# Kernel tuning notes

Hardware: AMD Instinct MI355X
Metric: run time of the kernel (lower is better)

Reference implementation:

```python
import jax, jax.numpy as jnp
import numpy as np

B, C, H, W = 2, 64, 48, 48
NH = 8
EPS = 1e-5


def conv2d(x, w, b=None, pad=0):
    out = jax.lax.conv_general_dilated(x, w, (1, 1), [(pad, pad), (pad, pad)],
                                       dimension_numbers=('NCHW', 'OIHW', 'NCHW'))
    return out if b is None else out + b[None, :, None, None]


def bn2d(x, g, b, m, v):
    # eval-mode BatchNorm2d with running stats
    return (x - m[None, :, None, None]) * (g / jnp.sqrt(v + EPS))[None, :, None, None] + b[None, :, None, None]


def ln(x, g, b):
    mu = x.mean(-1, keepdims=True)
    var = ((x - mu) ** 2).mean(-1, keepdims=True)
    return (x - mu) / jnp.sqrt(var + EPS) * g + b


def _forward(x, y, pconv_w, pconv_b, bnd_g, bnd_b, bnd_m, bnd_v,
             lnx_g, lnx_b, lny_g, lny_b, lnz_g, lnz_b,
             k_w, k_b, qv_w, qv_b, proj_w, proj_b,
             c2w1, c2b1, c2bn1_g, c2bn1_b, c2bn1_m, c2bn1_v,
             c2w2, c2b2, c2bn2_g, c2bn2_b, c2bn2_m, c2bn2_v,
             bn2_g, bn2_b, bn2_m, bn2_v,
             f1w, fbn1_g, fbn1_b, fbn1_m, fbn1_v,
             f2w, fbn2_g, fbn2_b, fbn2_m, fbn2_v,
             f3w, f3b):
    Bq, Cq, Hq, Wq = x.shape
    N = Hq * Wq
    hd = Cq // NH
    scale = hd ** -0.5
    xy = conv2d(jnp.concatenate([x, y], 1), pconv_w, pconv_b, pad=0)
    xb = bn2d(x, bnd_g, bnd_b, bnd_m, bnd_v)
    yb = bn2d(y, bnd_g, bnd_b, bnd_m, bnd_v)
    xyb = bn2d(xy, bnd_g, bnd_b, bnd_m, bnd_v)
    sc1 = xb.reshape(Bq, Cq, N).transpose(0, 2, 1)  # [B,N,C]
    sd1 = yb.reshape(Bq, Cq, N).transpose(0, 2, 1)
    xl = ln(sc1, lnx_g, lnx_b)
    yl = ln(sd1, lny_g, lny_b)
    zl = ln(xyb.reshape(Bq, Cq, N).transpose(0, 2, 1), lnz_g, lnz_b)

    def qv_heads(t):
        qv = (t @ qv_w.T + qv_b).reshape(Bq, N, 2, NH, hd)
        return qv[:, :, 0].transpose(0, 2, 1, 3), qv[:, :, 1].transpose(0, 2, 1, 3)

    x_q, x_v = qv_heads(xl)
    y_q, y_v = qv_heads(yl)
    k = (zl @ k_w.T + k_b).reshape(Bq, N, NH, hd).transpose(0, 2, 1, 3)  # [B,H,N,hd]
    attn1 = jnp.einsum('bhnd,bhmd->bhnm', x_q, k) * scale
    attn2 = jnp.einsum('bhnd,bhmd->bhnm', y_q, k) * scale
    attn = jax.nn.softmax(attn1 * attn2, axis=-1)  # product of two score maps
    xo = jnp.einsum('bhnm,bhmd->bhnd', attn, x_v).transpose(0, 2, 1, 3).reshape(Bq, N, Cq) @ proj_w.T + proj_b
    yo = jnp.einsum('bhnm,bhmd->bhnd', attn, y_v).transpose(0, 2, 1, 3).reshape(Bq, N, Cq) @ proj_w.T + proj_b
    xo = (xo + sc1).transpose(0, 2, 1).reshape(Bq, Cq, Hq, Wq)
    yo = (yo + sd1).transpose(0, 2, 1).reshape(Bq, Cq, Hq, Wq)

    def conv2_block(t):  # shared-weight conv2 applied to both branches
        h = jax.nn.relu(bn2d(conv2d(t, c2w1, c2b1, pad=1), c2bn1_g, c2bn1_b, c2bn1_m, c2bn1_v))
        return jax.nn.relu(bn2d(conv2d(h, c2w2, c2b2, pad=1), c2bn2_g, c2bn2_b, c2bn2_m, c2bn2_v))

    xo = conv2_block(xo) + xo
    yo = conv2_block(yo) + yo
    cat = jnp.concatenate([xo + yo, xo * yo], 1)  # [B,2C,H,W]
    f = bn2d(cat, bn2_g, bn2_b, bn2_m, bn2_v)
    f = jax.nn.relu(bn2d(conv2d(f, f1w, None, pad=1), fbn1_g, fbn1_b, fbn1_m, fbn1_v))
    f = jax.nn.relu(bn2d(conv2d(f, f2w, None, pad=1), fbn2_g, fbn2_b, fbn2_m, fbn2_v))
    f = conv2d(f, f3w, f3b, pad=0)
    return cat + f


def setup_inputs() -> dict:
    ks = iter(jax.random.split(jax.random.key(0), 64))

    def nrm(shape, s=0.05):
        return jax.random.normal(next(ks), shape, jnp.float32) * s

    def bn_params(c):
        return (1.0 + nrm((c,)), nrm((c,)), nrm((c,)),
                jax.random.uniform(next(ks), (c,), jnp.float32, 0.5, 1.5))

    d = {}
    d['x'] = jax.random.normal(next(ks), (B, C, H, W), jnp.float32)
    d['y'] = jax.random.normal(next(ks), (B, C, H, W), jnp.float32)
    d['pconv_w'] = nrm((C, 2 * C, 1, 1)); d['pconv_b'] = nrm((C,))
    d['bnd_g'], d['bnd_b'], d['bnd_m'], d['bnd_v'] = bn_params(C)
    d['lnx_g'] = 1.0 + nrm((C,)); d['lnx_b'] = nrm((C,))
    d['lny_g'] = 1.0 + nrm((C,)); d['lny_b'] = nrm((C,))
    d['lnz_g'] = 1.0 + nrm((C,)); d['lnz_b'] = nrm((C,))
    d['k_w'] = nrm((C, C)); d['k_b'] = nrm((C,))
    d['qv_w'] = nrm((2 * C, C)); d['qv_b'] = nrm((2 * C,))
    d['proj_w'] = nrm((C, C)); d['proj_b'] = nrm((C,))
    d['c2w1'] = nrm((C, C, 3, 3)); d['c2b1'] = nrm((C,))
    d['c2bn1_g'], d['c2bn1_b'], d['c2bn1_m'], d['c2bn1_v'] = bn_params(C)
    d['c2w2'] = nrm((C, C, 3, 3)); d['c2b2'] = nrm((C,))
    d['c2bn2_g'], d['c2bn2_b'], d['c2bn2_m'], d['c2bn2_v'] = bn_params(C)
    d['bn2_g'], d['bn2_b'], d['bn2_m'], d['bn2_v'] = bn_params(2 * C)
    d['f1w'] = nrm((2 * C, 2 * C, 3, 3))
    d['fbn1_g'], d['fbn1_b'], d['fbn1_m'], d['fbn1_v'] = bn_params(2 * C)
    d['f2w'] = nrm((2 * C, 2 * C, 3, 3))
    d['fbn2_g'], d['fbn2_b'], d['fbn2_m'], d['fbn2_v'] = bn_params(2 * C)
    d['f3w'] = nrm((2 * C, 2 * C, 1, 1)); d['f3b'] = nrm((2 * C,))
    return d


def reference(x, y, pconv_w, pconv_b, bnd_g, bnd_b, bnd_m, bnd_v,
              lnx_g, lnx_b, lny_g, lny_b, lnz_g, lnz_b,
              k_w, k_b, qv_w, qv_b, proj_w, proj_b,
              c2w1, c2b1, c2bn1_g, c2bn1_b, c2bn1_m, c2bn1_v,
              c2w2, c2b2, c2bn2_g, c2bn2_b, c2bn2_m, c2bn2_v,
              bn2_g, bn2_b, bn2_m, bn2_v,
              f1w, fbn1_g, fbn1_b, fbn1_m, fbn1_v,
              f2w, fbn2_g, fbn2_b, fbn2_m, fbn2_v,
              f3w, f3b):
    return _forward(x, y, pconv_w, pconv_b, bnd_g, bnd_b, bnd_m, bnd_v,
                    lnx_g, lnx_b, lny_g, lny_b, lnz_g, lnz_b,
                    k_w, k_b, qv_w, qv_b, proj_w, proj_b,
                    c2w1, c2b1, c2bn1_g, c2bn1_b, c2bn1_m, c2bn1_v,
                    c2w2, c2b2, c2bn2_g, c2bn2_b, c2bn2_m, c2bn2_v,
                    bn2_g, bn2_b, bn2_m, bn2_v,
                    f1w, fbn1_g, fbn1_b, fbn1_m, fbn1_v,
                    f2w, fbn2_g, fbn2_b, fbn2_m, fbn2_v,
                    f3w, f3b)
```

## Files before the change

### kernel.cpp

```cpp
#include <hip/hip_runtime.h>
#include <hip/hip_bf16.h>

#define B_   2
#define C_   64
#define H_   48
#define W_   48
#define N_   (H_*W_)
#define NH_  8
#define HD_  8
#define EPS_ 1e-5f
#define S2_  0.125f
#define LOG2E_ 1.44269504f
#define FS_  (S2_ * LOG2E_)
#define S_   ((size_t)B_ * C_ * N_)
#define CN_  ((size_t)C_ * N_)
#define ROWP_ 52
#define CBUF_ (8 * ROWP_)
#define XTSZ_ ((N_ + 2 * W_) * 128)

typedef unsigned short u16;
typedef __attribute__((ext_vector_type(8))) short short8v;
typedef __attribute__((ext_vector_type(4))) float f32x4;
union F8 { uint4 u4; short8v s; unsigned int w[4]; };

__device__ __forceinline__ float wsum64(float v) {
#pragma unroll
  for (int o = 32; o > 0; o >>= 1) v += __shfl_xor(v, o, 64);
  return v;
}

__device__ __forceinline__ float ln_val(float t, float g, float b) {
  float mu  = wsum64(t) * (1.0f / 64.0f);
  float d   = t - mu;
  float var = wsum64(d * d) * (1.0f / 64.0f);
  return d * rsqrtf(var + EPS_) * g + b;
}

__device__ __forceinline__ u16 f2bf(float x) {
  union { float f; unsigned int u; } a; a.f = x;
  unsigned int r = a.u + 0x7fffu + ((a.u >> 16) & 1u);
  return (u16)(r >> 16);
}

__global__ __launch_bounds__(1024) void k_pre(
    const float* __restrict__ x, const float* __restrict__ y,
    const float* __restrict__ pw, const float* __restrict__ pb,
    const float* g, const float* bb, const float* m, const float* v,
    const float* lnxg, const float* lnxb,
    const float* lnyg, const float* lnyb,
    const float* lnzg, const float* lnzb,
    float* __restrict__ xl, float* __restrict__ yl, float* __restrict__ zl) {
  __shared__ float4 pwT[32][64];
  __shared__ float xs[16][64], ys[16][64];
  int w = threadIdx.x >> 6, c = threadIdx.x & 63;
  for (int idx = threadIdx.x; idx < 2048; idx += 1024) {
    int cc = idx & 63, i4 = idx >> 6;
    pwT[i4][cc] = *(const float4*)(pw + (size_t)cc * 2 * C_ + i4 * 4);
  }
  int row = blockIdx.x * 16 + w;
  int b = row / N_, n = row % N_;
  float xv = x[(size_t)(b * C_ + c) * N_ + n];
  float yv = y[(size_t)(b * C_ + c) * N_ + n];
  xs[w][c] = xv; ys[w][c] = yv;
  __syncthreads();
  const float4* xw = (const float4*)xs[w];
  const float4* yw = (const float4*)ys[w];
  float acc = pb[c];
#pragma unroll
  for (int t = 0; t < 16; ++t) {
    float4 a = xw[t], wv = pwT[t][c];
    acc += a.x * wv.x + a.y * wv.y + a.z * wv.z + a.w * wv.w;
  }
#pragma unroll
  for (int t = 0; t < 16; ++t) {
    float4 a = yw[t], wv = pwT[16 + t][c];
    acc += a.x * wv.x + a.y * wv.y + a.z * wv.z + a.w * wv.w;
  }
  float s  = g[c] * rsqrtf(v[c] + EPS_);
  float sh = bb[c] - m[c] * s;
  float tx = xv * s + sh;
  xl[(size_t)row * C_ + c] = ln_val(tx, lnxg[c], lnxb[c]);
  float ty = yv * s + sh;
  yl[(size_t)row * C_ + c] = ln_val(ty, lnyg[c], lnyb[c]);
  float tz = acc * s + sh;
  zl[(size_t)row * C_ + c] = ln_val(tz, lnzg[c], lnzb[c]);
}

__global__ __launch_bounds__(64) void k_qvk(
    const float* __restrict__ xl, const float* __restrict__ yl,
    const float* __restrict__ zl,
    const float* __restrict__ qvw, const float* __restrict__ qvb,
    const float* __restrict__ kw, const float* __restrict__ kb,
    u16* __restrict__ qxb, u16* __restrict__ qyb,
    u16* __restrict__ kbf, u16* __restrict__ vt) {
  int l = threadIdx.x;
  int part = blockIdx.y >> 2;
  int j0 = (blockIdx.y & 3) * 16;
  int row = blockIdx.x * 64 + l;
  int b = row / N_, n = row % N_;
  const float* inp = (part < 2) ? xl : (part < 4) ? yl : zl;
  float4 in[16];
  const float4* ir = (const float4*)(inp + (size_t)row * C_);
#pragma unroll
  for (int t = 0; t < 16; ++t) in[t] = ir[t];

  const float* wb   = (part == 4) ? kw : qvw;
  const float* bias = (part == 4) ? kb : qvb;
  int joff = (part == 1 || part == 3) ? 64 : 0;

  if (part == 1 || part == 3) {
    int vbase = (part == 1) ? 0 : 8;
#pragma unroll
    for (int jj = 0; jj < 16; ++jj) {
      int j = j0 + jj;
      const float4* wr = (const float4*)(wb + (size_t)(joff + j) * C_);
      float acc = bias[joff + j];
#pragma unroll
      for (int t = 0; t < 16; ++t) {
        float4 a = in[t], wv = wr[t];
        acc += a.x * wv.x + a.y * wv.y + a.z * wv.z + a.w * wv.w;
      }
      int h = j >> 3, d = j & 7;
      vt[((size_t)((b * NH_ + h) * 16 + vbase + d)) * N_ + n] = f2bf(acc);
    }
  } else {
    u16* dst = (part == 0) ? qxb : (part == 2) ? qyb : kbf;
#pragma unroll
    for (int gg = 0; gg < 2; ++gg) {
      int h = (j0 >> 3) + gg;
      union { uint4 u4; u16 s[8]; } pk;
#pragma unroll
      for (int d = 0; d < 8; ++d) {
        int j = h * 8 + d;
        const float4* wr = (const float4*)(wb + (size_t)(joff + j) * C_);
        float acc = bias[joff + j];
#pragma unroll
        for (int t = 0; t < 16; ++t) {
          float4 a = in[t], wv = wr[t];
          acc += a.x * wv.x + a.y * wv.y + a.z * wv.z + a.w * wv.w;
        }
        if (part == 0) acc *= FS_;
        pk.s[d] = f2bf(acc);
      }
      *(uint4*)(dst + ((size_t)(b * NH_ + h) * N_ + n) * 8) = pk.u4;
    }
  }
}

__global__ __launch_bounds__(128, 5) void k_attn8(
    const u16* __restrict__ qx, const u16* __restrict__ qy,
    const u16* __restrict__ kk, const u16* __restrict__ vt,
    float* __restrict__ outx, float* __restrict__ outy) {
  __shared__ float sAcc[2][4][64];
  __shared__ float sL[2][16];
  int qt = blockIdx.x, bh = blockIdx.y;
  int tid = threadIdx.x;
  int lane = tid & 63;
  int wave = tid >> 6;
  int l15 = lane & 15;
  int q0 = qt * 16;

  F8 qxf, qyf;
  size_t qoff = ((size_t)bh * N_ + q0 + l15) * 8;
  qxf.u4 = *(const uint4*)(qx + qoff);
  qyf.u4 = *(const uint4*)(qy + qoff);
  if (lane >= 16) {
    qxf.u4 = make_uint4(0u, 0u, 0u, 0u);
    qyf.u4 = make_uint4(0u, 0u, 0u, 0u);
  }

  int key0 = wave * (N_ / 2);
  const uint4* kp = (const uint4*)(kk + (size_t)bh * N_ * 8) + key0 + l15;
  const uint4* vp = (const uint4*)(vt + ((size_t)bh * 16 + l15) * N_ + key0)
                    + (lane >> 4);
  int addr0 = (((lane >> 4) & 1) * 32 + l15) * 4;
  int addr1 = addr0 + 64;
  int thi = lane >> 5;

  f32x4 acc = {0.f, 0.f, 0.f, 0.f};
  const f32x4 z4 = {0.f, 0.f, 0.f, 0.f};
  float lsum = 0.f;

  F8 ka, kb2, vf;
  ka.u4 = kp[0]; kb2.u4 = kp[16]; vf.u4 = *vp;
  for (int c = 0; c < 36; ++c) {
    F8 kaC = ka, kbC = kb2, vfC = vf;
    kp += 32; vp += 4;
    ka.u4 = kp[0]; kb2.u4 = kp[16]; vf.u4 = *vp;

    f32x4 s1a = __builtin_amdgcn_mfma_f32_16x16x32_bf16(kaC.s, qxf.s, z4, 0, 0, 0);
    f32x4 s2a = __builtin_amdgcn_mfma_f32_16x16x32_bf16(kaC.s, qyf.s, z4, 0, 0, 0);
    f32x4 s1b = __builtin_amdgcn_mfma_f32_16x16x32_bf16(kbC.s, qxf.s, z4, 0, 0, 0);
    f32x4 s2b = __builtin_amdgcn_mfma_f32_16x16x32_bf16(kbC.s, qyf.s, z4, 0, 0, 0);

    float p00 = exp2f(s1a[0] * s2a[0]), p01 = exp2f(s1a[1] * s2a[1]);
    float p02 = exp2f(s1a[2] * s2a[2]), p03 = exp2f(s1a[3] * s2a[3]);
    float p10 = exp2f(s1b[0] * s2b[0]), p11 = exp2f(s1b[1] * s2b[1]);
    float p12 = exp2f(s1b[2] * s2b[2]), p13 = exp2f(s1b[3] * s2b[3]);
    lsum += ((p00 + p01) + (p02 + p03)) + ((p10 + p11) + (p12 + p13));

    unsigned int pk00, pk10, pk01, pk11;
    asm("v_cvt_pk_bf16_f32 %0, %1, %2" : "=v"(pk00) : "v"(p00), "v"(p01));
    asm("v_cvt_pk_bf16_f32 %0, %1, %2" : "=v"(pk10) : "v"(p02), "v"(p03));
    asm("v_cvt_pk_bf16_f32 %0, %1, %2" : "=v"(pk01) : "v"(p10), "v"(p11));
    asm("v_cvt_pk_bf16_f32 %0, %1, %2" : "=v"(pk11) : "v"(p12), "v"(p13));

    int b00 = __builtin_amdgcn_ds_bpermute(addr0, (int)pk00);
    int b01 = __builtin_amdgcn_ds_bpermute(addr0, (int)pk01);
    int b10 = __builtin_amdgcn_ds_bpermute(addr0, (int)pk10);
    int b11 = __builtin_amdgcn_ds_bpermute(addr0, (int)pk11);
    int c00 = __builtin_amdgcn_ds_bpermute(addr1, (int)pk00);
    int c01 = __builtin_amdgcn_ds_bpermute(addr1, (int)pk01);
    int c10 = __builtin_amdgcn_ds_bpermute(addr1, (int)pk10);
    int c11 = __builtin_amdgcn_ds_bpermute(addr1, (int)pk11);

    F8 pf;
    pf.w[0] = (unsigned int)(thi ? b01 : b00);
    pf.w[1] = (unsigned int)(thi ? b11 : b10);
    pf.w[2] = (unsigned int)(thi ? c01 : c00);
    pf.w[3] = (unsigned int)(thi ? c11 : c10);
    acc = __builtin_amdgcn_mfma_f32_16x16x32_bf16(pf.s, vfC.s, acc, 0, 0, 0);
  }

  lsum += __shfl_xor(lsum, 16, 64);
  lsum += __shfl_xor(lsum, 32, 64);
  if (lane < 16) sL[wave][lane] = lsum;
#pragma unroll
  for (int r = 0; r < 4; ++r) sAcc[wave][r][lane] = acc[r];
  __syncthreads();
  if (wave == 0) {
    float Linv = 1.f / (sL[0][l15] + sL[1][l15]);
    int b = bh >> 3, h = bh & 7;
    int d = l15 & 7;
    float* ob = (l15 < 8) ? outx : outy;
    size_t cbase = (size_t)b * N_ * C_ + (size_t)h * 8 + d;
#pragma unroll
    for (int r = 0; r < 4; ++r) {
      int qrow = 4 * (lane >> 4) + r;
      float li = __shfl(Linv, qrow, 64);
      float a = sAcc[0][r][lane] + sAcc[1][r][lane];
      ob[cbase + (size_t)(q0 + qrow) * C_] = a * li;
    }
  }
}

__global__ __launch_bounds__(64) void k_proj3(
    const float* __restrict__ attbase,
    const float* __restrict__ x, const float* __restrict__ y,
    const float* bg, const float* bb2, const float* bm, const float* bv,
    const float* __restrict__ pw, const float* __restrict__ pbias,
    float* __restrict__ outbase) {
  __shared__ float attT[64][66];
  int tid = threadIdx.x;
  int p0 = blockIdx.x * 64;
  int c0 = blockIdx.y * 2;
  int z = blockIdx.z;
  int branch = z >> 1, b = z & 1;
  const float* att = attbase + branch * S_ + (size_t)b * N_ * C_;
  for (int r = 0; r < 64; ++r)
    attT[tid][r] = att[(size_t)(p0 + r) * C_ + tid];
  __syncthreads();
  int p = p0 + tid;
  const float* w0 = pw + (size_t)c0 * C_;
  const float* w1 = w0 + C_;
  float a0 = pbias[c0], a1 = pbias[c0 + 1];
#pragma unroll 8
  for (int c = 0; c < C_; ++c) {
    float av = attT[c][tid];
    a0 += av * w0[c];
    a1 += av * w1[c];
  }
  float s0  = bg[c0] * rsqrtf(bv[c0] + EPS_);
  float sh0 = bb2[c0] - bm[c0] * s0;
  float s1  = bg[c0+1] * rsqrtf(bv[c0+1] + EPS_);
  float sh1 = bb2[c0+1] - bm[c0+1] * s1;
  const float* xin = branch ? y : x;
  float r0 = xin[((size_t)b * C_ + c0) * N_ + p];
  float r1 = xin[((size_t)b * C_ + c0 + 1) * N_ + p];
  size_t o = (size_t)z * CN_ + (size_t)c0 * N_ + p;
  outbase[o]      = a0 + r0 * s0 + sh0;
  outbase[o + N_] = a1 + r1 * s1 + sh1;
}

template<int CIN, int CIPB>
__device__ __forceinline__ void conv_core3(
    const float* __restrict__ ib, const float* __restrict__ w,
    int c0, int ci0, int p0, int tid, float (*bufs)[CBUF_],
    float4& A0, float4& A1) {
  const float* w0r = w + ((size_t)c0 * CIN + ci0) * 9;
  const float* w1r = w0r + (size_t)CIN * 9;
  int p  = p0 + tid * 4;
  int yy0 = p0 / W_;
  int yy = p / W_, x0 = p - yy * W_;
  int lr = yy - yy0;
  bool okL = x0 > 0, okR = x0 + 4 < W_;

  int rf0 = tid / 12, cf0 = tid - rf0 * 12;
  int gy0 = yy0 - 1 + rf0;
  int rf1 = (64 + tid) / 12, cf1 = (64 + tid) - rf1 * 12;
  int gy1 = yy0 - 1 + rf1;
  bool v0 = (unsigned)gy0 < (unsigned)H_;
  bool v1 = (tid < 32) && ((unsigned)gy1 < (unsigned)H_);
  int o0 = gy0 * W_ + cf0 * 4;
  int o1 = gy1 * W_ + cf1 * 4;
  int lo0 = rf0 * ROWP_ + cf0 * 4;
  int lo1 = rf1 * ROWP_ + cf1 * 4;
  const float4 zz = make_float4(0.f, 0.f, 0.f, 0.f);

  {
    const float* s = ib + (size_t)ci0 * N_;
    float4 ga = v0 ? *(const float4*)(s + o0) : zz;
    *(float4*)(&bufs[0][lo0]) = ga;
    if (tid < 32) {
      float4 gb = v1 ? *(const float4*)(s + o1) : zz;
      *(float4*)(&bufs[0][lo1]) = gb;
    }
  }
  float wc[18];
#pragma unroll
  for (int i = 0; i < 9; ++i) { wc[i] = w0r[i]; wc[9 + i] = w1r[i]; }

#pragma unroll 2
  for (int ci = 0; ci < CIPB; ++ci) {
    float4 ga = zz, gb = zz;
    float wn[18];
    if (ci + 1 < CIPB) {
      const float* s = ib + (size_t)(ci0 + ci + 1) * N_;
      ga = v0 ? *(const float4*)(s + o0) : zz;
      gb = v1 ? *(const float4*)(s + o1) : zz;
      const float* nw0 = w0r + (ci + 1) * 9;
      const float* nw1 = w1r + (ci + 1) * 9;
#pragma unroll
      for (int i = 0; i < 9; ++i) { wn[i] = nw0[i]; wn[9 + i] = nw1[i]; }
    }
    const float* bc = bufs[ci & 1];
#pragma unroll
    for (int ky = 0; ky < 3; ++ky) {
      int base = (lr + ky) * ROWP_ + x0;
      float4 mid = *(const float4*)(bc + base);
      float l = okL ? bc[base - 1] : 0.f;
      float r = okR ? bc[base + 4] : 0.f;
      float u0 = wc[ky*3], u1 = wc[ky*3+1], u2 = wc[ky*3+2];
      float t0 = wc[9+ky*3], t1 = wc[9+ky*3+1], t2 = wc[9+ky*3+2];
      A0.x += l     * u0 + mid.x * u1 + mid.y * u2;
      A0.y += mid.x * u0 + mid.y * u1 + mid.z * u2;
      A0.z += mid.y * u0 + mid.z * u1 + mid.w * u2;
      A0.w += mid.z * u0 + mid.w * u1 + r     * u2;
      A1.x += l     * t0 + mid.x * t1 + mid.y * t2;
      A1.y += mid.x * t0 + mid.y * t1 + mid.z * t2;
      A1.z += mid.y * t0 + mid.z * t1 + mid.w * t2;
      A1.w += mid.z * t0 + mid.w * t1 + r     * t2;
    }
    if (ci + 1 < CIPB) {
      float* d = bufs[(ci + 1) & 1];
      *(float4*)(&d[lo0]) = ga;
      if (tid < 32) *(float4*)(&d[lo1]) = gb;
#pragma unroll
      for (int i = 0; i < 18; ++i) wc[i] = wn[i];
    }
  }
}

template<int MODE>
__global__ __launch_bounds__(128) void k_convf(
    const float* __restrict__ inA, const float* __restrict__ inB,
    const float* __restrict__ w, const float* __restrict__ cb,
    const float* g, const float* b2, const float* m, const float* v,
    const float* __restrict__ resid,
    float* __restrict__ oA, float* __restrict__ oB) {
  __shared__ float lds[2 * 2 * CBUF_ + 512];
  int tid = threadIdx.x, wave = tid >> 6, lane = tid & 63;
  int tile = blockIdx.x, c0 = blockIdx.y * 2, img = blockIdx.z;
  const float* ib = (img < 2) ? inA + (size_t)img * CN_
                              : inB + (size_t)(img - 2) * CN_;
  float (*mybufs)[CBUF_] = (float(*)[CBUF_])(lds + wave * 2 * CBUF_);
  float* comb = lds + 4 * CBUF_;
  float4 A0 = make_float4(0.f,0.f,0.f,0.f);
  float4 A1 = make_float4(0.f,0.f,0.f,0.f);
  conv_core3<C_, C_/2>(ib, w, c0, wave * (C_/2), tile * 256, lane, mybufs,
                       A0, A1);
  float* cw = comb + wave * 256 + lane * 4;
  *(float4*)cw = wave ? A0 : A1;
  __syncthreads();
  {
    int c = c0 + wave;
    const float4 other = *(const float4*)(comb + (1 - wave) * 256 + lane * 4);
    float4 a = wave ? other : A0;
    float4 d = wave ? A1 : other;
    int p = tile * 256 + lane * 4;
    float s  = g[c] * rsqrtf(v[c] + EPS_);
    float sh = b2[c] - m[c] * s;
    float bias = cb[c];
    float4 r;
    r.x = fmaxf((a.x + d.x + bias) * s + sh, 0.f);
    r.y = fmaxf((a.y + d.y + bias) * s + sh, 0.f);
    r.z = fmaxf((a.z + d.z + bias) * s + sh, 0.f);
    r.w = fmaxf((a.w + d.w + bias) * s + sh, 0.f);
    size_t off = (size_t)img * CN_ + (size_t)c * N_ + p;
    if (MODE == 0) {
      float* ob = (img < 2) ? oA + off : oB + off - 2 * CN_;
      *(float4*)ob = r;
    } else {
      float4 rr = *(const float4*)(resid + off);
      r.x += rr.x; r.y += rr.y; r.z += rr.z; r.w += rr.w;
      *(float4*)(oA + off) = r;
    }
  }
}

__global__ void k_catbn(const float* __restrict__ o2,
                        const float* __restrict__ g, const float* __restrict__ b2,
                        const float* __restrict__ m, const float* __restrict__ v,
                        float* __restrict__ cat, u16* __restrict__ xt1) {
  int t = blockIdx.x * 256 + threadIdx.x;
  int p4 = t * 4;
  int n  = p4 % N_;
  int c2 = (p4 / N_) % (2 * C_);
  int b  = p4 / (2 * C_ * N_);
  int c  = c2 & 63;
  float4 X = *(const float4*)(o2 + (size_t)b * CN_ + (size_t)c * N_ + n);
  float4 Y = *(const float4*)(o2 + (size_t)(2 + b) * CN_ + (size_t)c * N_ + n);
  float4 val;
  if (c2 < C_) val = make_float4(X.x + Y.x, X.y + Y.y, X.z + Y.z, X.w + Y.w);
  else         val = make_float4(X.x * Y.x, X.y * Y.y, X.z * Y.z, X.w * Y.w);
  size_t co = ((size_t)b * 2 * C_ + c2) * N_ + n;
  *(float4*)(cat + co) = val;
  float s  = g[c2] * rsqrtf(v[c2] + EPS_);
  float sh = b2[c2] - m[c2] * s;
  u16* xb = xt1 + (size_t)b * XTSZ_ + (size_t)(W_ + n) * 128 + c2;
  xb[0]       = f2bf(val.x * s + sh);
  xb[128]     = f2bf(val.y * s + sh);
  xb[256]     = f2bf(val.z * s + sh);
  xb[384]     = f2bf(val.w * s + sh);
}

__global__ void k_zg(u16* __restrict__ xt1, u16* __restrict__ xt2) {
  int idx = blockIdx.x * 256 + threadIdx.x;
  if (idx >= 24576) return;
  int r = idx / 3072, o = idx - r * 3072;
  u16* base = (r & 4) ? xt2 : xt1;
  int b = (r >> 1) & 1, hi = r & 1;
  unsigned int* p = (unsigned int*)(base + (size_t)b * XTSZ_
                                    + (hi ? (size_t)(W_ + N_) * 128 : 0));
  p[o] = 0u;
}

__global__ void k_wcvt(const float* __restrict__ w1,
                       const float* __restrict__ w2,
                       u16* __restrict__ wb1, u16* __restrict__ wb2) {
  int idx = blockIdx.x * 256 + threadIdx.x;
  if (idx >= 2 * 147456) return;
  int layer = idx / 147456, rem = idx - layer * 147456;
  int t = rem / 16384, r2 = rem - t * 16384;
  int co = r2 >> 7, ci = r2 & 127;
  const float* w = layer ? w2 : w1;
  u16* ob = layer ? wb2 : wb1;
  ob[rem] = f2bf(w[(size_t)co * 1152 + ci * 9 + t]);
}

template<int MODE>
__global__ __launch_bounds__(64) void k_fmma(
    const u16* __restrict__ xt, const u16* __restrict__ wb,
    const float* g, const float* b2, const float* m, const float* v,
    u16* __restrict__ xto, float* __restrict__ fo) {
  int l = threadIdx.x;
  int c = l & 15, gg = l >> 4;
  int px0 = blockIdx.x * 16;
  int ct0 = blockIdx.y * 16;
  int b = blockIdx.z;
  int x0 = px0 % W_;
  bool mL = (x0 == 0) && (c == 0);
  bool mR = (x0 == 32) && (c == 15);
  const u16* xb = xt + (size_t)b * XTSZ_ + (size_t)W_ * 128;
  const u16* aw = wb + (size_t)(ct0 + c) * 128 + gg * 8;

  f32x4 acc = {0.f, 0.f, 0.f, 0.f};
#pragma unroll
  for (int cb = 0; cb < 4; ++cb) {
#pragma unroll
    for (int t = 0; t < 9; ++t) {
      const int dx = t % 3 - 1, dy = t / 3 - 1;
      F8 af, bf;
      af.u4 = *(const uint4*)(aw + t * 16384 + cb * 32);
      int px = px0 + c + dx + dy * W_;
      px = max(px, -W_);
      bf.u4 = *(const uint4*)(xb + (ptrdiff_t)px * 128 + cb * 32 + gg * 8);
      bool msk = (dx < 0 && mL) || (dx > 0 && mR);
      if (msk) bf.u4 = make_uint4(0u, 0u, 0u, 0u);
      acc = __builtin_amdgcn_mfma_f32_16x16x32_bf16(af.s, bf.s, acc, 0, 0, 0);
    }
  }
  int px = px0 + c;
  if (MODE == 0) {
    union { ushort4 u; u16 s[4]; } pk;
#pragma unroll
    for (int r = 0; r < 4; ++r) {
      int cout = ct0 + 4 * gg + r;
      float s = g[cout] * rsqrtf(v[cout] + EPS_);
      float sh = b2[cout] - m[cout] * s;
      pk.s[r] = f2bf(fmaxf(acc[r] * s + sh, 0.f));
    }
    *(ushort4*)(xto + (size_t)b * XTSZ_ + (size_t)(W_ + px) * 128
                + ct0 + 4 * gg) = pk.u;
  } else {
#pragma unroll
    for (int r = 0; r < 4; ++r) {
      int cout = ct0 + 4 * gg + r;
      fo[(size_t)b * S_ + (size_t)cout * N_ + px] = acc[r];
    }
  }
}

__global__ __launch_bounds__(64) void k_final3(
    const float* __restrict__ ff, size_t strideF,
    const float* __restrict__ g2, const float* __restrict__ b2,
    const float* __restrict__ m2, const float* __restrict__ v2,
    const float* __restrict__ cat,
    const float* __restrict__ w, const float* __restrict__ fb,
    float* __restrict__ out) {
  __shared__ float fsc[2 * C_], fsh[2 * C_];
  for (int j = threadIdx.x; j < 2 * C_; j += 64) {
    float s = g2[j] * rsqrtf(v2[j] + EPS_);
    fsc[j] = s;
    fsh[j] = b2[j] - m2[j] * s;
  }
  __syncthreads();
  int p = blockIdx.x * 128 + threadIdx.x * 2;
  int c0 = blockIdx.y * 2;
  int b = blockIdx.z;
  const float* fr = ff + (size_t)b * strideF;
  const float* wr0 = w + (size_t)c0 * 2 * C_;
  const float* wr1 = wr0 + 2 * C_;
  float a00 = fb[c0], a01 = a00;
  float a10 = fb[c0 + 1], a11 = a10;
#pragma unroll 4
  for (int j = 0; j < 2 * C_; ++j) {
    float2 fa = *(const float2*)(fr + (size_t)j * N_ + p);
    float s = fsc[j], sh = fsh[j];
    float f0 = fmaxf(fa.x * s + sh, 0.f);
    float f1 = fmaxf(fa.y * s + sh, 0.f);
    float wv0 = wr0[j], wv1 = wr1[j];
    a00 += wv0 * f0; a01 += wv0 * f1;
    a10 += wv1 * f0; a11 += wv1 * f1;
  }
  size_t o = ((size_t)b * 2 * C_ + c0) * N_ + p;
  float2 cv0 = *(const float2*)(cat + o);
  float2 cv1 = *(const float2*)(cat + o + N_);
  *(float2*)(out + o)      = make_float2(a00 + cv0.x, a01 + cv0.y);
  *(float2*)(out + o + N_) = make_float2(a10 + cv1.x, a11 + cv1.y);
}

extern "C" void kernel_launch(void* const* d_in, const int* in_sizes, int n_in,
                              void* d_out, int out_size, void* d_ws, size_t ws_size,
                              hipStream_t stream) {
  const float* x       = (const float*)d_in[0];
  const float* y       = (const float*)d_in[1];
  const float* pconv_w = (const float*)d_in[2];
  const float* pconv_b = (const float*)d_in[3];
  const float* bnd_g = (const float*)d_in[4];
  const float* bnd_b = (const float*)d_in[5];
  const float* bnd_m = (const float*)d_in[6];
  const float* bnd_v = (const float*)d_in[7];
  const float* lnx_g = (const float*)d_in[8];
  const float* lnx_b = (const float*)d_in[9];
  const float* lny_g = (const float*)d_in[10];
  const float* lny_b = (const float*)d_in[11];
  const float* lnz_g = (const float*)d_in[12];
  const float* lnz_b = (const float*)d_in[13];
  const float* k_w   = (const float*)d_in[14];
  const float* k_b   = (const float*)d_in[15];
  const float* qv_w  = (const float*)d_in[16];
  const float* qv_b  = (const float*)d_in[17];
  const float* proj_w = (const float*)d_in[18];
  const float* proj_b = (const float*)d_in[19];
  const float* c2w1  = (const float*)d_in[20];
  const float* c2b1  = (const float*)d_in[21];
  const float* c2bn1_g = (const float*)d_in[22];
  const float* c2bn1_b = (const float*)d_in[23];
  const float* c2bn1_m = (const float*)d_in[24];
  const float* c2bn1_v = (const float*)d_in[25];
  const float* c2w2  = (const float*)d_in[26];
  const float* c2b2  = (const float*)d_in[27];
  const float* c2bn2_g = (const float*)d_in[28];
  const float* c2bn2_b = (const float*)d_in[29];
  const float* c2bn2_m = (const float*)d_in[30];
  const float* c2bn2_v = (const float*)d_in[31];
  const float* bn2_g = (const float*)d_in[32];
  const float* bn2_b = (const float*)d_in[33];
  const float* bn2_m = (const float*)d_in[34];
  const float* bn2_v = (const float*)d_in[35];
  const float* f1w   = (const float*)d_in[36];
  const float* fbn1_g = (const float*)d_in[37];
  const float* fbn1_b = (const float*)d_in[38];
  const float* fbn1_m = (const float*)d_in[39];
  const float* fbn1_v = (const float*)d_in[40];
  const float* f2w   = (const float*)d_in[41];
  const float* fbn2_g = (const float*)d_in[42];
  const float* fbn2_b = (const float*)d_in[43];
  const float* fbn2_m = (const float*)d_in[44];
  const float* fbn2_v = (const float*)d_in[45];
  const float* f3w   = (const float*)d_in[46];
  const float* f3b   = (const float*)d_in[47];

  float* ws = (float*)d_ws;
  float* sl0 = ws + 0 * S_;
  float* sl1 = ws + 1 * S_;
  float* sl2 = ws + 2 * S_;
  float* sl3 = ws + 3 * S_;
  float* sl4 = ws + 4 * S_;
  float* sl5 = ws + 5 * S_;
  float* sl7 = ws + 7 * S_;
  u16* xt1  = (u16*)sl5;
  u16* xt2  = (u16*)sl0;
  u16* wbf1 = (u16*)sl7;
  u16* wbf2 = wbf1 + 9 * 16384;
  float* f2o = sl5;

  k_pre<<<B_ * N_ / 16, 1024, 0, stream>>>(x, y, pconv_w, pconv_b,
                                    bnd_g, bnd_b, bnd_m, bnd_v,
                                    lnx_g, lnx_b, lny_g, lny_b, lnz_g, lnz_b,
                                    sl1, sl2, sl3);
  u16* qxb = (u16*)(ws + 4 * S_);
  u16* qyb = qxb + (size_t)B_ * NH_ * N_ * 8;
  u16* kbf = (u16*)sl5;
  u16* vtb = (u16*)(ws + 6 * S_);
  {
    dim3 g(B_ * N_ / 64, 20);
    k_qvk<<<g, 64, 0, stream>>>(sl1, sl2, sl3, qv_w, qv_b, k_w, k_b,
                                qxb, qyb, kbf, vtb);
  }
  {
    dim3 g(N_ / 16, B_ * NH_);
    k_attn8<<<g, 128, 0, stream>>>(qxb, qyb, kbf, vtb, sl1, sl2);
  }
  {
    dim3 g(36, C_ / 2, 2 * B_);
    k_proj3<<<g, 64, 0, stream>>>(sl1, x, y, bnd_g, bnd_b, bnd_m, bnd_v,
                                  proj_w, proj_b, sl3);
  }
  {
    dim3 g(9, C_ / 2, 4);
    k_convf<0><<<g, 128, 0, stream>>>(sl3, sl3 + 2 * CN_, c2w1, c2b1,
        c2bn1_g, c2bn1_b, c2bn1_m, c2bn1_v, sl3, sl0, sl7);
  }
  {
    dim3 g(9, C_ / 2, 4);
    k_convf<1><<<g, 128, 0, stream>>>(sl0, sl7, c2w2, c2b2,
        c2bn2_g, c2bn2_b, c2bn2_m, c2bn2_v, sl3, sl1, sl1);
  }
  k_wcvt<<<1152, 256, 0, stream>>>(f1w, f2w, wbf1, wbf2);
  k_catbn<<<576, 256, 0, stream>>>(sl1, bn2_g, bn2_b, bn2_m, bn2_v,
                                   sl3, xt1);
  k_zg<<<96, 256, 0, stream>>>(xt1, xt2);
  {
    dim3 g(N_ / 16, 8, B_);
    k_fmma<0><<<g, 64, 0, stream>>>(xt1, wbf1,
        fbn1_g, fbn1_b, fbn1_m, fbn1_v, xt2, nullptr);
    k_fmma<1><<<g, 64, 0, stream>>>(xt2, wbf2,
        nullptr, nullptr, nullptr, nullptr, nullptr, f2o);
  }
  {
    dim3 g(18, C_, B_);
    k_final3<<<g, 64, 0, stream>>>(f2o, S_,
                                   fbn2_g, fbn2_b, fbn2_m, fbn2_v,
                                   sl3, f3w, f3b, (float*)d_out);
  }
}
```

Before: 357.1 us.

## Run conv2 3x3 convolutions as bf16 MFMA implicit GEMMs instead of FP32 direct conv

Replaces the FP32 direct-convolution kernels for the two 64-channel 3x3 convs with the existing bf16 MFMA implicit-GEMM kernel, adding modes for bias+BN+ReLU and for the residual output. The projection kernel now also writes a padded bf16 channels-last copy of its output for the first conv, and weight conversion for all four convs is merged into one kernel launched early. This targets the FP32 FMA cost of the direct conv, at the price of bf16 rounding in the conv path and more workspace aliasing.

```diff
diff --git a/kernel.cpp b/kernel.cpp
--- a/kernel.cpp
+++ b/kernel.cpp
@@ -14,9 +14,8 @@
 #define FS_  (S2_ * LOG2E_)
 #define S_   ((size_t)B_ * C_ * N_)
 #define CN_  ((size_t)C_ * N_)
-#define ROWP_ 52
-#define CBUF_ (8 * ROWP_)
-#define XTSZ_ ((N_ + 2 * W_) * 128)
+#define XTSZ_ ((size_t)(N_ + 2 * W_) * 128)
+#define XTSC_ ((size_t)(N_ + 2 * W_) * 64)
 
 typedef unsigned short u16;
 typedef __attribute__((ext_vector_type(8))) short short8v;
@@ -244,12 +243,12 @@
   }
 }
 
-__global__ __launch_bounds__(64) void k_proj3(
+__global__ __launch_bounds__(64) void k_proj4(
     const float* __restrict__ attbase,
     const float* __restrict__ x, const float* __restrict__ y,
     const float* bg, const float* bb2, const float* bm, const float* bv,
     const float* __restrict__ pw, const float* __restrict__ pbias,
-    float* __restrict__ outbase) {
+    float* __restrict__ outbase, u16* __restrict__ xt0) {
   __shared__ float attT[64][66];
   int tid = threadIdx.x;
   int p0 = blockIdx.x * 64;
@@ -277,135 +276,13 @@
   const float* xin = branch ? y : x;
   float r0 = xin[((size_t)b * C_ + c0) * N_ + p];
   float r1 = xin[((size_t)b * C_ + c0 + 1) * N_ + p];
+  float v0 = a0 + r0 * s0 + sh0;
+  float v1 = a1 + r1 * s1 + sh1;
   size_t o = (size_t)z * CN_ + (size_t)c0 * N_ + p;
-  outbase[o]      = a0 + r0 * s0 + sh0;
-  outbase[o + N_] = a1 + r1 * s1 + sh1;
-}
-
-template<int CIN, int CIPB>
-__device__ __forceinline__ void conv_core3(
-    const float* __restrict__ ib, const float* __restrict__ w,
-    int c0, int ci0, int p0, int tid, float (*bufs)[CBUF_],
-    float4& A0, float4& A1) {
-  const float* w0r = w + ((size_t)c0 * CIN + ci0) * 9;
-  const float* w1r = w0r + (size_t)CIN * 9;
-  int p  = p0 + tid * 4;
-  int yy0 = p0 / W_;
-  int yy = p / W_, x0 = p - yy * W_;
-  int lr = yy - yy0;
-  bool okL = x0 > 0, okR = x0 + 4 < W_;
-
-  int rf0 = tid / 12, cf0 = tid - rf0 * 12;
-  int gy0 = yy0 - 1 + rf0;
-  int rf1 = (64 + tid) / 12, cf1 = (64 + tid) - rf1 * 12;
-  int gy1 = yy0 - 1 + rf1;
-  bool v0 = (unsigned)gy0 < (unsigned)H_;
-  bool v1 = (tid < 32) && ((unsigned)gy1 < (unsigned)H_);
-  int o0 = gy0 * W_ + cf0 * 4;
-  int o1 = gy1 * W_ + cf1 * 4;
-  int lo0 = rf0 * ROWP_ + cf0 * 4;
-  int lo1 = rf1 * ROWP_ + cf1 * 4;
-  const float4 zz = make_float4(0.f, 0.f, 0.f, 0.f);
-
-  {
-    const float* s = ib + (size_t)ci0 * N_;
-    float4 ga = v0 ? *(const float4*)(s + o0) : zz;
-    *(float4*)(&bufs[0][lo0]) = ga;
-    if (tid < 32) {
-      float4 gb = v1 ? *(const float4*)(s + o1) : zz;
-      *(float4*)(&bufs[0][lo1]) = gb;
-    }
-  }
-  float wc[18];
-#pragma unroll
-  for (int i = 0; i < 9; ++i) { wc[i] = w0r[i]; wc[9 + i] = w1r[i]; }
-
-#pragma unroll 2
-  for (int ci = 0; ci < CIPB; ++ci) {
-    float4 ga = zz, gb = zz;
-    float wn[18];
-    if (ci + 1 < CIPB) {
-      const float* s = ib + (size_t)(ci0 + ci + 1) * N_;
-      ga = v0 ? *(const float4*)(s + o0) : zz;
-      gb = v1 ? *(const float4*)(s + o1) : zz;
-      const float* nw0 = w0r + (ci + 1) * 9;
-      const float* nw1 = w1r + (ci + 1) * 9;
-#pragma unroll
-      for (int i = 0; i < 9; ++i) { wn[i] = nw0[i]; wn[9 + i] = nw1[i]; }
-    }
-    const float* bc = bufs[ci & 1];
-#pragma unroll
-    for (int ky = 0; ky < 3; ++ky) {
-      int base = (lr + ky) * ROWP_ + x0;
-      float4 mid = *(const float4*)(bc + base);
-      float l = okL ? bc[base - 1] : 0.f;
-      float r = okR ? bc[base + 4] : 0.f;
-      float u0 = wc[ky*3], u1 = wc[ky*3+1], u2 = wc[ky*3+2];
-      float t0 = wc[9+ky*3], t1 = wc[9+ky*3+1], t2 = wc[9+ky*3+2];
-      A0.x += l     * u0 + mid.x * u1 + mid.y * u2;
-      A0.y += mid.x * u0 + mid.y * u1 + mid.z * u2;
-      A0.z += mid.y * u0 + mid.z * u1 + mid.w * u2;
-      A0.w += mid.z * u0 + mid.w * u1 + r     * u2;
-      A1.x += l     * t0 + mid.x * t1 + mid.y * t2;
-      A1.y += mid.x * t0 + mid.y * t1 + mid.z * t2;
-      A1.z += mid.y * t0 + mid.z * t1 + mid.w * t2;
-      A1.w += mid.z * t0 + mid.w * t1 + r     * t2;
-    }
-    if (ci + 1 < CIPB) {
-      float* d = bufs[(ci + 1) & 1];
-      *(float4*)(&d[lo0]) = ga;
-      if (tid < 32) *(float4*)(&d[lo1]) = gb;
-#pragma unroll
-      for (int i = 0; i < 18; ++i) wc[i] = wn[i];
-    }
-  }
-}
-
-template<int MODE>
-__global__ __launch_bounds__(128) void k_convf(
-    const float* __restrict__ inA, const float* __restrict__ inB,
-    const float* __restrict__ w, const float* __restrict__ cb,
-    const float* g, const float* b2, const float* m, const float* v,
-    const float* __restrict__ resid,
-    float* __restrict__ oA, float* __restrict__ oB) {
-  __shared__ float lds[2 * 2 * CBUF_ + 512];
-  int tid = threadIdx.x, wave = tid >> 6, lane = tid & 63;
-  int tile = blockIdx.x, c0 = blockIdx.y * 2, img = blockIdx.z;
-  const float* ib = (img < 2) ? inA + (size_t)img * CN_
-                              : inB + (size_t)(img - 2) * CN_;
-  float (*mybufs)[CBUF_] = (float(*)[CBUF_])(lds + wave * 2 * CBUF_);
-  float* comb = lds + 4 * CBUF_;
-  float4 A0 = make_float4(0.f,0.f,0.f,0.f);
-  float4 A1 = make_float4(0.f,0.f,0.f,0.f);
-  conv_core3<C_, C_/2>(ib, w, c0, wave * (C_/2), tile * 256, lane, mybufs,
-                       A0, A1);
-  float* cw = comb + wave * 256 + lane * 4;
-  *(float4*)cw = wave ? A0 : A1;
-  __syncthreads();
-  {
-    int c = c0 + wave;
-    const float4 other = *(const float4*)(comb + (1 - wave) * 256 + lane * 4);
-    float4 a = wave ? other : A0;
-    float4 d = wave ? A1 : other;
-    int p = tile * 256 + lane * 4;
-    float s  = g[c] * rsqrtf(v[c] + EPS_);
-    float sh = b2[c] - m[c] * s;
-    float bias = cb[c];
-    float4 r;
-    r.x = fmaxf((a.x + d.x + bias) * s + sh, 0.f);
-    r.y = fmaxf((a.y + d.y + bias) * s + sh, 0.f);
-    r.z = fmaxf((a.z + d.z + bias) * s + sh, 0.f);
-    r.w = fmaxf((a.w + d.w + bias) * s + sh, 0.f);
-    size_t off = (size_t)img * CN_ + (size_t)c * N_ + p;
-    if (MODE == 0) {
-      float* ob = (img < 2) ? oA + off : oB + off - 2 * CN_;
-      *(float4*)ob = r;
-    } else {
-      float4 rr = *(const float4*)(resid + off);
-      r.x += rr.x; r.y += rr.y; r.z += rr.z; r.w += rr.w;
-      *(float4*)(oA + off) = r;
-    }
-  }
+  outbase[o]      = v0;
+  outbase[o + N_] = v1;
+  unsigned int pv = ((unsigned int)f2bf(v1) << 16) | (unsigned int)f2bf(v0);
+  *(unsigned int*)(xt0 + (size_t)z * XTSC_ + (size_t)(W_ + p) * 64 + c0) = pv;
 }
 
 __global__ void k_catbn(const float* __restrict__ o2,
@@ -428,41 +305,62 @@
   float s  = g[c2] * rsqrtf(v[c2] + EPS_);
   float sh = b2[c2] - m[c2] * s;
   u16* xb = xt1 + (size_t)b * XTSZ_ + (size_t)(W_ + n) * 128 + c2;
-  xb[0]       = f2bf(val.x * s + sh);
-  xb[128]     = f2bf(val.y * s + sh);
-  xb[256]     = f2bf(val.z * s + sh);
-  xb[384]     = f2bf(val.w * s + sh);
-}
-
-__global__ void k_zg(u16* __restrict__ xt1, u16* __restrict__ xt2) {
+  xb[0]   = f2bf(val.x * s + sh);
+  xb[128] = f2bf(val.y * s + sh);
+  xb[256] = f2bf(val.z * s + sh);
+  xb[384] = f2bf(val.w * s + sh);
+}
+
+__global__ void k_zg(u16* __restrict__ b0, u16* __restrict__ b1,
+                     int nimg, int cinc) {
+  int gsz = W_ * cinc / 2;
+  int pbt = nimg * 2 * gsz;
   int idx = blockIdx.x * 256 + threadIdx.x;
-  if (idx >= 24576) return;
-  int r = idx / 3072, o = idx - r * 3072;
-  u16* base = (r & 4) ? xt2 : xt1;
-  int b = (r >> 1) & 1, hi = r & 1;
-  unsigned int* p = (unsigned int*)(base + (size_t)b * XTSZ_
-                                    + (hi ? (size_t)(W_ + N_) * 128 : 0));
-  p[o] = 0u;
+  if (idx >= 2 * pbt) return;
+  u16* base = (idx < pbt) ? b0 : b1;
+  int r = idx % pbt;
+  int img = r / (2 * gsz);
+  int r2 = r % (2 * gsz);
+  int hi = r2 / gsz, o = r2 % gsz;
+  size_t xts = (size_t)(N_ + 2 * W_) * cinc;
+  ((unsigned int*)(base + (size_t)img * xts
+                   + (hi ? (size_t)(W_ + N_) * cinc : 0)))[o] = 0u;
 }
 
 __global__ void k_wcvt(const float* __restrict__ w1,
                        const float* __restrict__ w2,
-                       u16* __restrict__ wb1, u16* __restrict__ wb2) {
+                       const float* __restrict__ cw1,
+                       const float* __restrict__ cw2,
+                       u16* __restrict__ wb) {
   int idx = blockIdx.x * 256 + threadIdx.x;
-  if (idx >= 2 * 147456) return;
-  int layer = idx / 147456, rem = idx - layer * 147456;
-  int t = rem / 16384, r2 = rem - t * 16384;
-  int co = r2 >> 7, ci = r2 & 127;
-  const float* w = layer ? w2 : w1;
-  u16* ob = layer ? wb2 : wb1;
-  ob[rem] = f2bf(w[(size_t)co * 1152 + ci * 9 + t]);
+  if (idx >= 368640) return;
+  if (idx < 294912) {
+    int layer = idx / 147456, rem = idx - layer * 147456;
+    int t = rem / 16384, r2 = rem - t * 16384;
+    int co = r2 >> 7, ci = r2 & 127;
+    wb[idx] = f2bf((layer ? w2 : w1)[(size_t)co * 1152 + ci * 9 + t]);
+  } else {
+    int k = idx - 294912;
+    int layer = k / 36864, rem = k - layer * 36864;
+    int t = rem / 4096, r2 = rem - t * 4096;
+    int co = r2 >> 6, ci = r2 & 63;
+    wb[idx] = f2bf((layer ? cw2 : cw1)[(size_t)co * 576 + ci * 9 + t]);
+  }
 }
 
 template<int MODE>
 __global__ __launch_bounds__(64) void k_fmma(
     const u16* __restrict__ xt, const u16* __restrict__ wb,
+    const float* __restrict__ cbias,
     const float* g, const float* b2, const float* m, const float* v,
+    const float* __restrict__ resid,
     u16* __restrict__ xto, float* __restrict__ fo) {
+  constexpr int CIN  = (MODE >= 2) ? 64 : 128;
+  constexpr int NCB  = CIN / 32;
+  constexpr int COUT = (MODE >= 2) ? 64 : 128;
+  constexpr int TS   = CIN * COUT;
+  constexpr size_t XTS = (size_t)(N_ + 2 * W_) * CIN;
+  constexpr size_t XTSO = (size_t)(N_ + 2 * W_) * COUT;
   int l = threadIdx.x;
   int c = l & 15, gg = l >> 4;
   int px0 = blockIdx.x * 16;
@@ -471,42 +369,53 @@
   int x0 = px0 % W_;
   bool mL = (x0 == 0) && (c == 0);
   bool mR = (x0 == 32) && (c == 15);
-  const u16* xb = xt + (size_t)b * XTSZ_ + (size_t)W_ * 128;
-  const u16* aw = wb + (size_t)(ct0 + c) * 128 + gg * 8;
+  const u16* xb = xt + (size_t)b * XTS + (size_t)W_ * CIN;
+  const u16* aw = wb + (size_t)(ct0 + c) * CIN + gg * 8;
 
   f32x4 acc = {0.f, 0.f, 0.f, 0.f};
 #pragma unroll
-  for (int cb = 0; cb < 4; ++cb) {
+  for (int cb = 0; cb < NCB; ++cb) {
 #pragma unroll
     for (int t = 0; t < 9; ++t) {
       const int dx = t % 3 - 1, dy = t / 3 - 1;
       F8 af, bf;
-      af.u4 = *(const uint4*)(aw + t * 16384 + cb * 32);
+      af.u4 = *(const uint4*)(aw + t * TS + cb * 32);
       int px = px0 + c + dx + dy * W_;
       px = max(px, -W_);
-      bf.u4 = *(const uint4*)(xb + (ptrdiff_t)px * 128 + cb * 32 + gg * 8);
+      bf.u4 = *(const uint4*)(xb + (ptrdiff_t)px * CIN + cb * 32 + gg * 8);
       bool msk = (dx < 0 && mL) || (dx > 0 && mR);
       if (msk) bf.u4 = make_uint4(0u, 0u, 0u, 0u);
       acc = __builtin_amdgcn_mfma_f32_16x16x32_bf16(af.s, bf.s, acc, 0, 0, 0);
     }
   }
   int px = px0 + c;
-  if (MODE == 0) {
+  if (MODE == 0 || MODE == 2) {
     union { ushort4 u; u16 s[4]; } pk;
 #pragma unroll
     for (int r = 0; r < 4; ++r) {
       int cout = ct0 + 4 * gg + r;
+      float a = acc[r] + (MODE == 2 ? cbias[cout] : 0.f);
       float s = g[cout] * rsqrtf(v[cout] + EPS_);
       float sh = b2[cout] - m[cout] * s;
-      pk.s[r] = f2bf(fmaxf(acc[r] * s + sh, 0.f));
-    }
-    *(ushort4*)(xto + (size_t)b * XTSZ_ + (size_t)(W_ + px) * 128
+      pk.s[r] = f2bf(fmaxf(a * s + sh, 0.f));
+    }
+    *(ushort4*)(xto + (size_t)b * XTSO + (size_t)(W_ + px) * COUT
                 + ct0 + 4 * gg) = pk.u;
-  } else {
+  } else if (MODE == 1) {
 #pragma unroll
     for (int r = 0; r < 4; ++r) {
       int cout = ct0 + 4 * gg + r;
       fo[(size_t)b * S_ + (size_t)cout * N_ + px] = acc[r];
+    }
+  } else {
+#pragma unroll
+    for (int r = 0; r < 4; ++r) {
+      int cout = ct0 + 4 * gg + r;
+      float a = acc[r] + cbias[cout];
+      float s = g[cout] * rsqrtf(v[cout] + EPS_);
+      float sh = b2[cout] - m[cout] * s;
+      size_t off = (size_t)b * CN_ + (size_t)cout * N_ + px;
+      fo[off] = fmaxf(a * s + sh, 0.f) + resid[off];
     }
   }
 }
@@ -603,23 +512,28 @@
   const float* f3b   = (const float*)d_in[47];
 
   float* ws = (float*)d_ws;
-  float* sl0 = ws + 0 * S_;
   float* sl1 = ws + 1 * S_;
   float* sl2 = ws + 2 * S_;
   float* sl3 = ws + 3 * S_;
-  float* sl4 = ws + 4 * S_;
   float* sl5 = ws + 5 * S_;
-  float* sl7 = ws + 7 * S_;
-  u16* xt1  = (u16*)sl5;
-  u16* xt2  = (u16*)sl0;
-  u16* wbf1 = (u16*)sl7;
-  u16* wbf2 = wbf1 + 9 * 16384;
+  u16* xtC0 = (u16*)sl5;
+  u16* xtC1 = (u16*)ws;
+  u16* xtF1 = (u16*)(ws + 3 * S_ / 2);
+  u16* xtF2 = (u16*)ws;
+  float* xo4 = sl3;
+  float* o2  = sl5;
   float* f2o = sl5;
+  u16* wb   = (u16*)(ws + 7 * S_);
+  u16* wbf1 = wb;
+  u16* wbf2 = wb + 147456;
+  u16* wbc1 = wb + 294912;
+  u16* wbc2 = wb + 331776;
 
   k_pre<<<B_ * N_ / 16, 1024, 0, stream>>>(x, y, pconv_w, pconv_b,
                                     bnd_g, bnd_b, bnd_m, bnd_v,
                                     lnx_g, lnx_b, lny_g, lny_b, lnz_g, lnz_b,
                                     sl1, sl2, sl3);
+  k_wcvt<<<1440, 256, 0, stream>>>(f1w, f2w, c2w1, c2w2, wb);
   u16* qxb = (u16*)(ws + 4 * S_);
   u16* qyb = qxb + (size_t)B_ * NH_ * N_ * 8;
   u16* kbf = (u16*)sl5;
@@ -635,29 +549,29 @@
   }
   {
     dim3 g(36, C_ / 2, 2 * B_);
-    k_proj3<<<g, 64, 0, stream>>>(sl1, x, y, bnd_g, bnd_b, bnd_m, bnd_v,
-                                  proj_w, proj_b, sl3);
-  }
-  {
-    dim3 g(9, C_ / 2, 4);
-    k_convf<0><<<g, 128, 0, stream>>>(sl3, sl3 + 2 * CN_, c2w1, c2b1,
-        c2bn1_g, c2bn1_b, c2bn1_m, c2bn1_v, sl3, sl0, sl7);
-  }
-  {
-    dim3 g(9, C_ / 2, 4);
-    k_convf<1><<<g, 128, 0, stream>>>(sl0, sl7, c2w2, c2b2,
-        c2bn2_g, c2bn2_b, c2bn2_m, c2bn2_v, sl3, sl1, sl1);
-  }
-  k_wcvt<<<1152, 256, 0, stream>>>(f1w, f2w, wbf1, wbf2);
-  k_catbn<<<576, 256, 0, stream>>>(sl1, bn2_g, bn2_b, bn2_m, bn2_v,
-                                   sl3, xt1);
-  k_zg<<<96, 256, 0, stream>>>(xt1, xt2);
+    k_proj4<<<g, 64, 0, stream>>>(sl1, x, y, bnd_g, bnd_b, bnd_m, bnd_v,
+                                  proj_w, proj_b, xo4, xtC0);
+  }
+  k_zg<<<96, 256, 0, stream>>>(xtC0, xtC1, 4, 64);
+  {
+    dim3 g(N_ / 16, 4, 4);
+    k_fmma<2><<<g, 64, 0, stream>>>(xtC0, wbc1, c2b1,
+        c2bn1_g, c2bn1_b, c2bn1_m, c2bn1_v, nullptr, xtC1, nullptr);
+  }
+  {
+    dim3 g(N_ / 16, 4, 4);
+    k_fmma<3><<<g, 64, 0, stream>>>(xtC1, wbc2, c2b2,
+        c2bn2_g, c2bn2_b, c2bn2_m, c2bn2_v, xo4, nullptr, o2);
+  }
+  k_zg<<<96, 256, 0, stream>>>(xtF1, xtF2, 2, 128);
+  k_catbn<<<576, 256, 0, stream>>>(o2, bn2_g, bn2_b, bn2_m, bn2_v,
+                                   sl3, xtF1);
   {
     dim3 g(N_ / 16, 8, B_);
-    k_fmma<0><<<g, 64, 0, stream>>>(xt1, wbf1,
-        fbn1_g, fbn1_b, fbn1_m, fbn1_v, xt2, nullptr);
-    k_fmma<1><<<g, 64, 0, stream>>>(xt2, wbf2,
-        nullptr, nullptr, nullptr, nullptr, nullptr, f2o);
+    k_fmma<0><<<g, 64, 0, stream>>>(xtF1, wbf1, nullptr,
+        fbn1_g, fbn1_b, fbn1_m, fbn1_v, nullptr, xtF2, nullptr);
+    k_fmma<1><<<g, 64, 0, stream>>>(xtF2, wbf2, nullptr,
+        nullptr, nullptr, nullptr, nullptr, nullptr, nullptr, f2o);
   }
   {
     dim3 g(18, C_, B_);
```

New measurement: 321.8 us. 9.9% less time.
